# Kernel optimization log

Hardware: AMD Instinct MI355X
Metric: run time of the kernel (lower is better)

Reference implementation:

```python
import math
import jax, jax.numpy as jnp
import numpy as np

LOG_K = 9          # log_kernel_size
SIGMA_MIN = 0.5
SIGMA_MAX = 10.0


def setup_inputs() -> dict:
    key = jax.random.key(0)
    k1, k2 = jax.random.split(key)
    B, C, H, W = 4, 3, 256, 256
    x = jax.random.normal(k1, (B, C, H, W), dtype=jnp.float32)
    # foa_xy holds (x, y) pixel coordinates of the focus of attention
    foa_xy = jax.random.uniform(k2, (B, 2), dtype=jnp.float32) * jnp.array([W - 1, H - 1], jnp.float32)
    return {"x": x, "foa_xy": foa_xy}


def _log_per_pixel_kernels(foa_xy, H, W, k, sigma_min, sigma_max):
    """Per-pixel LoG kernels, shape [B, k*k, H*W] (out_ch=in_ch=1 spatial-only)."""
    B = foa_xy.shape[0]
    kk = k * k
    # pixel coordinate grid (x, y), flattened row-major: [HW, 2]
    yy, xx = jnp.meshgrid(jnp.arange(H), jnp.arange(W), indexing="ij")
    xx_yy = jnp.stack([xx.ravel(), yy.ravel()], axis=-1).astype(jnp.float32)
    # squared distances within the kernel window: [kk]
    r = jnp.arange(-(k // 2), k // 2 + 1)
    ryy, rxx = jnp.meshgrid(r, r, indexing="ij")
    r_sq = (rxx ** 2 + ryy ** 2).reshape(-1).astype(jnp.float32)
    # distance of every pixel from the FOA: [B, HW]
    diff = xx_yy[None, :, :] - foa_xy[:, None, :]
    dists = jnp.sqrt(jnp.sum(diff ** 2, axis=-1))
    diag = math.sqrt(H * H + W * W)
    dn = dists / diag
    sigma = (1.0 - dn) * sigma_min + dn * sigma_max        # linear sigma, [B, HW]
    s = sigma[:, None, :]                                   # [B, 1, HW]
    tmp = r_sq[None, :, None] / (2.0 * s * s)               # [B, kk, HW]
    factor = -1.0 / (math.pi * s ** 4)
    kern = factor * (1.0 - tmp) * jnp.exp(-tmp)
    kern = kern * jnp.sqrt(s)                               # scale_factor = sigma**0.5
    kern = kern * dists[:, None, :]                         # distance modulation
    return kern                                             # [B, kk, HW]


def reference(x, foa_xy):
    B, C, H, W = x.shape
    k = LOG_K
    pad = ((k - 1) * 1 + 1) // 2                            # dilation=1 -> 4
    xp = jnp.pad(x, ((0, 0), (0, 0), (pad, pad), (pad, pad)), mode="reflect")
    # im2col: [B, C*kk, H, W], feature dim ordered (channel-major, then kernel pos)
    patches = jax.lax.conv_general_dilated_patches(xp, (k, k), (1, 1), "VALID")
    patches = patches.reshape(B, C, k * k, H * W)
    kern = _log_per_pixel_kernels(foa_xy, H, W, k, SIGMA_MIN, SIGMA_MAX)  # [B, kk, HW]
    # spatial-only kernel: sum over kernel-area dim, broadcast over channels
    out = jnp.einsum("bckp,bkp->bcp", patches, kern)
    return out.reshape(B, C, H, W)
```

## Files before the change

### kernel.cpp

```cpp
#include <hip/hip_runtime.h>
#include <math.h>

#define HH 256
#define WW 256
#define CC 3
#define HW (HH*WW)

__global__ __launch_bounds__(256) void adaptive_log_kernel(
    const float* __restrict__ x, const float* __restrict__ foa,
    float* __restrict__ out)
{
    const int p  = blockIdx.x * 256 + threadIdx.x;
    const int b  = blockIdx.y;
    const int py = p >> 8;
    const int px = p & (WW - 1);

    const float fx = foa[2*b + 0];
    const float fy = foa[2*b + 1];
    const float ddx = (float)px - fx;
    const float ddy = (float)py - fy;
    const float dist = sqrtf(ddx*ddx + ddy*ddy);
    const float inv_diag = 1.0f / 362.03867196751236f;
    const float dn = dist * inv_diag;
    const float sigma = 0.5f + 9.5f * dn;
    const float s2 = sigma * sigma;
    const float inv2s2 = 0.5f / s2;
    const float factor = -1.0f / ((float)M_PI * s2 * s2);
    const float common = factor * sqrtf(sigma) * dist;

    float w[33];
    const int r2v[16] = {0,1,2,4,5,8,9,10,13,16,17,18,20,25,26,32};
    #pragma unroll
    for (int i = 0; i < 16; ++i) {
        const float t = (float)r2v[i] * inv2s2;
        w[r2v[i]] = common * (1.0f - t) * __expf(-t);
    }

    int xi[9], yi[9];
    #pragma unroll
    for (int i = 0; i < 9; ++i) {
        int xx = px + i - 4;
        xx = (xx < 0) ? -xx : xx;
        xx = (xx > WW-1) ? (2*(WW-1) - xx) : xx;
        xi[i] = xx;
        int yy = py + i - 4;
        yy = (yy < 0) ? -yy : yy;
        yy = (yy > HH-1) ? (2*(HH-1) - yy) : yy;
        yi[i] = yy * WW;
    }

    const float* xb = x + (size_t)b * (CC*HW);
    float a0 = 0.f, a1 = 0.f, a2 = 0.f;
    #pragma unroll
    for (int a = 0; a < 9; ++a) {
        const int dy = a - 4;
        #pragma unroll
        for (int bb = 0; bb < 9; ++bb) {
            const int dx = bb - 4;
            const float wv = w[dy*dy + dx*dx];
            const int off = yi[a] + xi[bb];
            a0 += wv * xb[off];
            a1 += wv * xb[off + HW];
            a2 += wv * xb[off + 2*HW];
        }
    }

    float* ob = out + (size_t)b * (CC*HW);
    ob[p]          = a0;
    ob[p + HW]     = a1;
    ob[p + 2*HW]   = a2;
}

extern "C" void kernel_launch(void* const* d_in, const int* in_sizes, int n_in,
                              void* d_out, int out_size, void* d_ws, size_t ws_size,
                              hipStream_t stream) {
    const float* x   = (const float*)d_in[0];
    const float* foa = (const float*)d_in[1];
    float* out = (float*)d_out;

    dim3 grid(HW / 256, 4);
    dim3 block(256);
    adaptive_log_kernel<<<grid, block, 0, stream>>>(x, foa, out);
}
```

Measured before the change: 64.29 us.

## Stage reflected input tiles in LDS and compute two pixels per thread

Each 256-thread block now loads a 64x8 output tile plus a 4-pixel reflected halo for all three channels into shared memory, then each thread computes two adjacent output pixels from vectorized float2 LDS reads. This replaces the 243 scattered global loads per pixel with shared-memory reuse. The per-pixel Gaussian exponentials are replaced by powers of a single exp(-1/(2s^2)), using the fact that every r^2 is an integer. The costs are the halo reload overhead (72x16 input per 64x8 output), more registers for two weight sets, and a grid of 512 blocks, which may underfill the GPU.

```diff
diff --git a/kernel.cpp b/kernel.cpp
--- a/kernel.cpp
+++ b/kernel.cpp
@@ -6,69 +6,123 @@
 #define CC 3
 #define HW (HH*WW)
 
+#define TW 64
+#define TH 8
+#define IW 72
+#define IH 16
+#define LDS_CH (IW*IH)
+#define LDS_TOT (LDS_CH*CC)
+
+__device__ __forceinline__ int reflect(int v, int n) {
+    v = (v < 0) ? -v : v;
+    v = (v > n - 1) ? (2 * (n - 1) - v) : v;
+    return v;
+}
+
+__device__ __forceinline__ constexpr int r2idx(int r2) {
+    switch (r2) {
+        case 0:  return 0;  case 1:  return 1;  case 2:  return 2;  case 4:  return 3;
+        case 5:  return 4;  case 8:  return 5;  case 9:  return 6;  case 10: return 7;
+        case 13: return 8;  case 16: return 9;  case 17: return 10; case 18: return 11;
+        case 20: return 12; case 25: return 13; case 26: return 14; default: return 15;
+    }
+}
+
 __global__ __launch_bounds__(256) void adaptive_log_kernel(
     const float* __restrict__ x, const float* __restrict__ foa,
     float* __restrict__ out)
 {
-    const int p  = blockIdx.x * 256 + threadIdx.x;
+    __shared__ float lds[LDS_TOT];
+    const int tid = threadIdx.x;
+    const int bx = blockIdx.x & 3;
+    const int by = blockIdx.x >> 2;
     const int b  = blockIdx.y;
-    const int py = p >> 8;
-    const int px = p & (WW - 1);
 
-    const float fx = foa[2*b + 0];
-    const float fy = foa[2*b + 1];
-    const float ddx = (float)px - fx;
-    const float ddy = (float)py - fy;
-    const float dist = sqrtf(ddx*ddx + ddy*ddy);
-    const float inv_diag = 1.0f / 362.03867196751236f;
-    const float dn = dist * inv_diag;
-    const float sigma = 0.5f + 9.5f * dn;
-    const float s2 = sigma * sigma;
-    const float inv2s2 = 0.5f / s2;
-    const float factor = -1.0f / ((float)M_PI * s2 * s2);
-    const float common = factor * sqrtf(sigma) * dist;
+    const int gx0 = bx * TW;
+    const int gy0 = by * TH;
 
-    float w[33];
-    const int r2v[16] = {0,1,2,4,5,8,9,10,13,16,17,18,20,25,26,32};
+    const float* xb = x + (size_t)b * (CC * HW);
+    for (int i = tid; i < LDS_TOT; i += 256) {
+        int c   = i / LDS_CH;
+        int rem = i - c * LDS_CH;
+        int r   = rem / IW;
+        int col = rem - r * IW;
+        int gr = reflect(gy0 + r - 4, HH);
+        int gc = reflect(gx0 + col - 4, WW);
+        lds[i] = xb[c * HW + gr * WW + gc];
+    }
+    __syncthreads();
+
+    const int tx = tid & 31;
+    const int ty = tid >> 5;
+
+    const int px0 = gx0 + tx * 2;
+    const int py  = gy0 + ty;
+
+    const float fx = foa[2 * b + 0];
+    const float fy = foa[2 * b + 1];
+
+    float w0[16], w1[16];
     #pragma unroll
-    for (int i = 0; i < 16; ++i) {
-        const float t = (float)r2v[i] * inv2s2;
-        w[r2v[i]] = common * (1.0f - t) * __expf(-t);
+    for (int o = 0; o < 2; ++o) {
+        float* w = o ? w1 : w0;
+        const float ddx = (float)(px0 + o) - fx;
+        const float ddy = (float)py - fy;
+        const float dist = sqrtf(ddx * ddx + ddy * ddy);
+        const float dn = dist * (1.0f / 362.03867196751236f);
+        const float sigma = 0.5f + 9.5f * dn;
+        const float s2 = sigma * sigma;
+        const float inv2s2 = 0.5f / s2;
+        const float common = (-1.0f / (float)M_PI) / (s2 * s2) * sqrtf(sigma) * dist;
+        const float q  = __expf(-inv2s2);
+        const float q2 = q * q;
+        const float q4 = q2 * q2;
+        const float q8 = q4 * q4;
+        const float q16 = q8 * q8;
+        float e[16];
+        e[0] = 1.0f;      e[1] = q;          e[2] = q2;         e[3] = q4;
+        e[4] = q4 * q;    e[5] = q8;         e[6] = q8 * q;     e[7] = q8 * q2;
+        e[8] = q8 * q4 * q;            e[9] = q16;        e[10] = q16 * q;
+        e[11] = q16 * q2; e[12] = q16 * q4;  e[13] = q16 * q8 * q;
+        e[14] = q16 * q8 * q2;         e[15] = q16 * q16;
+        const float r2v[16] = {0,1,2,4,5,8,9,10,13,16,17,18,20,25,26,32};
+        #pragma unroll
+        for (int k = 0; k < 16; ++k)
+            w[k] = common * (1.0f - r2v[k] * inv2s2) * e[k];
     }
 
-    int xi[9], yi[9];
+    float acc0[CC] = {0.f, 0.f, 0.f};
+    float acc1[CC] = {0.f, 0.f, 0.f};
     #pragma unroll
-    for (int i = 0; i < 9; ++i) {
-        int xx = px + i - 4;
-        xx = (xx < 0) ? -xx : xx;
-        xx = (xx > WW-1) ? (2*(WW-1) - xx) : xx;
-        xi[i] = xx;
-        int yy = py + i - 4;
-        yy = (yy < 0) ? -yy : yy;
-        yy = (yy > HH-1) ? (2*(HH-1) - yy) : yy;
-        yi[i] = yy * WW;
-    }
-
-    const float* xb = x + (size_t)b * (CC*HW);
-    float a0 = 0.f, a1 = 0.f, a2 = 0.f;
-    #pragma unroll
-    for (int a = 0; a < 9; ++a) {
-        const int dy = a - 4;
+    for (int c = 0; c < CC; ++c) {
         #pragma unroll
-        for (int bb = 0; bb < 9; ++bb) {
-            const int dx = bb - 4;
-            const float wv = w[dy*dy + dx*dx];
-            const int off = yi[a] + xi[bb];
-            a0 += wv * xb[off];
-            a1 += wv * xb[off + HW];
-            a2 += wv * xb[off + 2*HW];
+        for (int i = 0; i < 9; ++i) {
+            const float2* row = (const float2*)&lds[c * LDS_CH + (ty + i) * IW + tx * 2];
+            const float2 f01 = row[0];
+            const float2 f23 = row[1];
+            const float2 f45 = row[2];
+            const float2 f67 = row[3];
+            const float2 f89 = row[4];
+            const float f[10] = {f01.x, f01.y, f23.x, f23.y, f45.x,
+                                 f45.y, f67.x, f67.y, f89.x, f89.y};
+            const int dy2 = (i - 4) * (i - 4);
+            float s0 = 0.f, s1 = 0.f;
+            #pragma unroll
+            for (int m = 0; m < 9; ++m) {
+                const int dx2 = (m - 4) * (m - 4);
+                s0 += w0[r2idx(dy2 + dx2)] * f[m];
+                s1 += w1[r2idx(dy2 + dx2)] * f[m + 1];
+            }
+            acc0[c] += s0;
+            acc1[c] += s1;
         }
     }
 
-    float* ob = out + (size_t)b * (CC*HW);
-    ob[p]          = a0;
-    ob[p + HW]     = a1;
-    ob[p + 2*HW]   = a2;
+    float* ob = out + (size_t)b * (CC * HW) + py * WW + px0;
+    #pragma unroll
+    for (int c = 0; c < CC; ++c) {
+        *(float2*)&ob[c * HW] = make_float2(acc0[c], acc1[c]);
+    }
 }
 
 extern "C" void kernel_launch(void* const* d_in, const int* in_sizes, int n_in,
@@ -78,7 +132,7 @@
     const float* foa = (const float*)d_in[1];
     float* out = (float*)d_out;
 
-    dim3 grid(HW / 256, 4);
+    dim3 grid(4 * 32, 4);
     dim3 block(256);
     adaptive_log_kernel<<<grid, block, 0, stream>>>(x, foa, out);
 }
```

After: 65.24 us. About the same (+1.5%).
